# Kernel tuning notes

Hardware: AMD Instinct MI355X
Metric: run time of the kernel (lower is better)

## Reference

```python
import jax, jax.numpy as jnp
import numpy as np

EPS = 1e-5
DOWNSAMPLE = 0.5


def setup_inputs() -> dict:
    key = jax.random.key(0)
    k1, k2, k3 = jax.random.split(key, 3)
    B, C, H, W = 32, 256, 128, 128
    x = jax.random.normal(k1, (B, C, H, W), dtype=jnp.float32)
    # 1x1 conv: weight [3, C], bias [3]
    conv_w = jax.random.normal(k2, (3, C), dtype=jnp.float32) / np.sqrt(C).astype(np.float32)
    conv_b = jax.random.normal(k3, (3,), dtype=jnp.float32) * 0.01
    return {"x": x, "conv_w": conv_w, "conv_b": conv_b}


def reference(x, conv_w, conv_b):
    B, C, H, W = x.shape
    dh = int(round(H * DOWNSAMPLE))
    dw = int(round(W * DOWNSAMPLE))

    # 1x1 conv producing 3 channels: 2 offset + 1 attention logit
    oa = jnp.einsum('bchw,oc->bohw', x, conv_w) + conv_b[None, :, None, None]
    offset = oa[:, :2]                      # [B,2,H,W]
    attention = jnp.exp(oa[:, 2:3])         # [B,1,H,W]

    # normalized destination coordinates = base grid + offset, clamped
    gy = jnp.broadcast_to((jnp.arange(H, dtype=x.dtype) / H)[:, None], (H, W))
    gx = jnp.broadcast_to((jnp.arange(W, dtype=x.dtype) / W)[None, :], (H, W))
    base = jnp.stack([gy, gx])              # [2,H,W]
    dest = jnp.clip(base[None] + offset, 0.0, 1.0 - EPS)
    dy = jnp.floor(dest[:, 0] * dh)
    dx = jnp.floor(dest[:, 1] * dw)
    cell = (dy * dw + dx).astype(jnp.int32)  # [B,H,W] spatial cell index

    # full flat destination index over (batch, channel, cell)
    b_off = jnp.arange(B, dtype=jnp.int32)[:, None, None, None] * (C * dh * dw)
    c_off = jnp.arange(C, dtype=jnp.int32)[None, :, None, None] * (dh * dw)
    destination = cell[:, None] + b_off + c_off  # [B,C,H,W]

    # scatter-add attention-weighted features
    xw = (x * attention).reshape(-1)
    feat = jax.ops.segment_sum(xw, destination.reshape(-1), num_segments=B * C * dh * dw)

    # scatter-add attention per (batch, cell) for normalization
    a_idx = cell + jnp.arange(B, dtype=jnp.int32)[:, None, None] * (dh * dw)
    att_sum = jax.ops.segment_sum(attention.reshape(-1), a_idx.reshape(-1), num_segments=B * dh * dw) + EPS

    out = feat.reshape(B, C, dh, dw) / att_sum.reshape(B, 1, dh, dw)
    return (out, offset, destination)
```

## Files before the change

kernel.cpp:

```cpp
#include <hip/hip_runtime.h>
#include <math.h>

#define NB 32
#define NC 256
#define NH 128
#define NW 128
#define NDH 64
#define NDW 64
#define NHW (NH * NW)
#define NCELLS (NDH * NDW)
#define OUT0_N (NB * NC * NCELLS)
#define OUT1_BASE OUT0_N
#define OUT1_N (NB * 2 * NHW)
#define OUT2_BASE (OUT1_BASE + OUT1_N)

#define EPSF 1e-5f

typedef unsigned short u16;
typedef unsigned int   u32;

#define WS_CELLS     ((size_t)0)
#define WS_ATTBF     (WS_CELLS + (size_t)NB*NHW*2)
#define WS_ECOMB     (WS_ATTBF + (size_t)NB*NHW*2)
#define WS_IASUM     (WS_ECOMB + (size_t)NB*NHW*4)
#define WS_BASE_NEED (WS_IASUM + (size_t)NB*NCELLS*4)
#define WS_XATT      WS_BASE_NEED
#define WS_XATT_NEED (WS_XATT + (size_t)NB*NC*NHW*2)

__device__ __forceinline__ u16 f32_to_bf16_rn(float f) {
    const u32 u = __float_as_uint(f);
    return (u16)((u + 0x7FFFu + ((u >> 16) & 1u)) >> 16);
}

__device__ __forceinline__ void async_stage16(const void* g, void* l) {
    __builtin_amdgcn_global_load_lds(
        (const __attribute__((address_space(1))) unsigned int*)g,
        (__attribute__((address_space(3))) unsigned int*)l,
        16, 0, 0);
}

__global__ __launch_bounds__(256) void k_conv_x(
    const float* __restrict__ x, const float* __restrict__ cw,
    const float* __restrict__ cb, float* __restrict__ out,
    u16* __restrict__ cells, u16* __restrict__ attbf, u16* __restrict__ xatt)
{
    __shared__ float cwS[3][NC];
    __shared__ float red[256][13];
    __shared__ float attv[64];
    __shared__ int   cellv[64];

    const int t    = threadIdx.x;
    const int blk  = blockIdx.x;
    const int b    = blk >> 8;
    const int tile = blk & 255;
    const int h    = tile >> 1;
    const int w0   = (tile & 1) << 6;
    const int pixbase = h * NW + w0;

    cwS[0][t] = cw[t];
    cwS[1][t] = cw[NC + t];
    cwS[2][t] = cw[2 * NC + t];
    __syncthreads();

    const int ct = t >> 4;
    const int pg = (t & 15) << 2;
    const float* xb = x + (size_t)b * NC * NHW + pixbase + pg;

    float4 xr[16];
    float p00 = 0, p01 = 0, p02 = 0;
    float p10 = 0, p11 = 0, p12 = 0;
    float p20 = 0, p21 = 0, p22 = 0;
    float p30 = 0, p31 = 0, p32 = 0;

    #pragma unroll
    for (int i = 0; i < 16; ++i) {
        const int c = (i << 4) + ct;
        const float4 xv = *reinterpret_cast<const float4*>(xb + (size_t)c * NHW);
        xr[i] = xv;
        const float wc0 = cwS[0][c], wc1 = cwS[1][c], wc2 = cwS[2][c];
        p00 += xv.x * wc0; p01 += xv.x * wc1; p02 += xv.x * wc2;
        p10 += xv.y * wc0; p11 += xv.y * wc1; p12 += xv.y * wc2;
        p20 += xv.z * wc0; p21 += xv.z * wc1; p22 += xv.z * wc2;
        p30 += xv.w * wc0; p31 += xv.w * wc1; p32 += xv.w * wc2;
    }

    red[t][0]  = p00; red[t][1]  = p01; red[t][2]  = p02;
    red[t][3]  = p10; red[t][4]  = p11; red[t][5]  = p12;
    red[t][6]  = p20; red[t][7]  = p21; red[t][8]  = p22;
    red[t][9]  = p30; red[t][10] = p31; red[t][11] = p32;
    __syncthreads();

    if (t < 64) {
        const int px   = t;
        const int row0 = px >> 2;
        const int col  = (px & 3) * 3;
        float s0 = 0, s1 = 0, s2 = 0;
        #pragma unroll
        for (int j = 0; j < 16; ++j) {
            const int r = row0 + (j << 4);
            s0 += red[r][col];
            s1 += red[r][col + 1];
            s2 += red[r][col + 2];
        }
        const float off0 = s0 + cb[0];
        const float off1 = s1 + cb[1];
        const float att  = expf(s2 + cb[2]);

        const float gy = (float)h * (1.0f / NH);
        const float gx = (float)(w0 + px) * (1.0f / NW);
        const float dyf = fminf(fmaxf(gy + off0, 0.0f), 0.99999f);
        const float dxf = fminf(fmaxf(gx + off1, 0.0f), 0.99999f);
        const int dy = (int)floorf(dyf * (float)NDH);
        const int dx = (int)floorf(dxf * (float)NDW);
        const int cell = dy * NDW + dx;

        cellv[px] = cell;
        attv[px]  = att;
        cells[b * NHW + pixbase + px] = (u16)cell;
        attbf[b * NHW + pixbase + px] = f32_to_bf16_rn(att);

        const int o1 = OUT1_BASE + b * 2 * NHW + pixbase + px;
        out[o1]       = off0;
        out[o1 + NHW] = off1;
    }
    __syncthreads();

    const int  c0 = cellv[pg], c1 = cellv[pg + 1], c2 = cellv[pg + 2], c3 = cellv[pg + 3];
    const float a0 = attv[pg], a1 = attv[pg + 1], a2 = attv[pg + 2], a3 = attv[pg + 3];
    float* __restrict__ dst = out + OUT2_BASE;

    #pragma unroll
    for (int i = 0; i < 16; ++i) {
        const int c = (i << 4) + ct;
        const int basec = (b * NC + c) * NCELLS;
        float4 dv;
        dv.x = (float)(basec + c0);
        dv.y = (float)(basec + c1);
        dv.z = (float)(basec + c2);
        dv.w = (float)(basec + c3);
        *reinterpret_cast<float4*>(dst + (size_t)(b * NC + c) * NHW + pixbase + pg) = dv;

        const float4 xv = xr[i];
        const u32 lo = (u32)f32_to_bf16_rn(xv.x * a0)
                     | ((u32)f32_to_bf16_rn(xv.y * a1) << 16);
        const u32 hi = (u32)f32_to_bf16_rn(xv.z * a2)
                     | ((u32)f32_to_bf16_rn(xv.w * a3) << 16);
        *reinterpret_cast<uint2*>(xatt + (size_t)(b * NC + c) * NHW + pixbase + pg)
            = make_uint2(lo, hi);
    }
}

__global__ __launch_bounds__(256) void k_conv(
    const float* __restrict__ x, const float* __restrict__ cw,
    const float* __restrict__ cb, float* __restrict__ out,
    u16* __restrict__ cells, u16* __restrict__ attbf)
{
    __shared__ float cwS[3][NC];
    __shared__ float red[256][13];
    __shared__ int   cellv[64];

    const int t    = threadIdx.x;
    const int blk  = blockIdx.x;
    const int b    = blk >> 8;
    const int tile = blk & 255;
    const int h    = tile >> 1;
    const int w0   = (tile & 1) << 6;
    const int pixbase = h * NW + w0;

    cwS[0][t] = cw[t];
    cwS[1][t] = cw[NC + t];
    cwS[2][t] = cw[2 * NC + t];
    __syncthreads();

    const int ct = t >> 4;
    const int pg = (t & 15) << 2;
    const float* xb = x + (size_t)b * NC * NHW + pixbase + pg;

    float p00 = 0, p01 = 0, p02 = 0;
    float p10 = 0, p11 = 0, p12 = 0;
    float p20 = 0, p21 = 0, p22 = 0;
    float p30 = 0, p31 = 0, p32 = 0;

    #pragma unroll
    for (int i = 0; i < 16; ++i) {
        const int c = (i << 4) + ct;
        const float4 xv = *reinterpret_cast<const float4*>(xb + (size_t)c * NHW);
        const float wc0 = cwS[0][c], wc1 = cwS[1][c], wc2 = cwS[2][c];
        p00 += xv.x * wc0; p01 += xv.x * wc1; p02 += xv.x * wc2;
        p10 += xv.y * wc0; p11 += xv.y * wc1; p12 += xv.y * wc2;
        p20 += xv.z * wc0; p21 += xv.z * wc1; p22 += xv.z * wc2;
        p30 += xv.w * wc0; p31 += xv.w * wc1; p32 += xv.w * wc2;
    }

    red[t][0]  = p00; red[t][1]  = p01; red[t][2]  = p02;
    red[t][3]  = p10; red[t][4]  = p11; red[t][5]  = p12;
    red[t][6]  = p20; red[t][7]  = p21; red[t][8]  = p22;
    red[t][9]  = p30; red[t][10] = p31; red[t][11] = p32;
    __syncthreads();

    if (t < 64) {
        const int px   = t;
        const int row0 = px >> 2;
        const int col  = (px & 3) * 3;
        float s0 = 0, s1 = 0, s2 = 0;
        #pragma unroll
        for (int j = 0; j < 16; ++j) {
            const int r = row0 + (j << 4);
            s0 += red[r][col];
            s1 += red[r][col + 1];
            s2 += red[r][col + 2];
        }
        const float off0 = s0 + cb[0];
        const float off1 = s1 + cb[1];
        const float att  = expf(s2 + cb[2]);
        const float gy = (float)h * (1.0f / NH);
        const float gx = (float)(w0 + px) * (1.0f / NW);
        const float dyf = fminf(fmaxf(gy + off0, 0.0f), 0.99999f);
        const float dxf = fminf(fmaxf(gx + off1, 0.0f), 0.99999f);
        const int dy = (int)floorf(dyf * (float)NDH);
        const int dx = (int)floorf(dxf * (float)NDW);
        const int cell = dy * NDW + dx;
        cellv[px] = cell;
        cells[b * NHW + pixbase + px] = (u16)cell;
        attbf[b * NHW + pixbase + px] = f32_to_bf16_rn(att);
        const int o1 = OUT1_BASE + b * 2 * NHW + pixbase + px;
        out[o1]       = off0;
        out[o1 + NHW] = off1;
    }
    __syncthreads();

    const int  c0 = cellv[pg], c1 = cellv[pg + 1], c2 = cellv[pg + 2], c3 = cellv[pg + 3];
    float* __restrict__ dst = out + OUT2_BASE;
    #pragma unroll
    for (int i = 0; i < 16; ++i) {
        const int c = (i << 4) + ct;
        const int basec = (b * NC + c) * NCELLS;
        float4 dv;
        dv.x = (float)(basec + c0);
        dv.y = (float)(basec + c1);
        dv.z = (float)(basec + c2);
        dv.w = (float)(basec + c3);
        *reinterpret_cast<float4*>(dst + (size_t)(b * NC + c) * NHW + pixbase + pg) = dv;
    }
}

__global__ __launch_bounds__(1024) void k_sort(
    const u16* __restrict__ cells, const u16* __restrict__ attbf,
    u32* __restrict__ ecomb, float* __restrict__ iasum)
{
    __shared__ u32   hist[NCELLS];
    __shared__ float as_[NCELLS];
    __shared__ u32   ts[1024];

    const int t = threadIdx.x;
    const int b = blockIdx.x;
    const u16* cb_ = cells + b * NHW;
    const u16* ab_ = attbf + b * NHW;

    #pragma unroll
    for (int j = 0; j < 4; ++j) { hist[t + 1024 * j] = 0u; as_[t + 1024 * j] = 0.f; }
    __syncthreads();

    #pragma unroll
    for (int j = 0; j < 16; ++j) {
        const int p  = t + 1024 * j;
        const int cl = cb_[p];
        atomicAdd(&hist[cl], 1u);
        atomicAdd(&as_[cl], __uint_as_float((u32)ab_[p] << 16));
    }
    __syncthreads();

    const u32 h0 = hist[4 * t], h1 = hist[4 * t + 1], h2 = hist[4 * t + 2], h3 = hist[4 * t + 3];
    const u32 T  = h0 + h1 + h2 + h3;
    ts[t] = T;
    __syncthreads();
    for (int off = 1; off < 1024; off <<= 1) {
        const u32 v = (t >= off) ? ts[t - off] : 0u;
        __syncthreads();
        ts[t] += v;
        __syncthreads();
    }
    const u32 base = ts[t] - T;
    hist[4 * t]     = base;
    hist[4 * t + 1] = base + h0;
    hist[4 * t + 2] = base + h0 + h1;
    hist[4 * t + 3] = base + h0 + h1 + h2;

    #pragma unroll
    for (int j = 0; j < 4; ++j) {
        const int i = t + 1024 * j;
        iasum[b * NCELLS + i] = 1.0f / (as_[i] + EPSF);
    }
    __syncthreads();

    #pragma unroll
    for (int j = 0; j < 16; ++j) {
        const int p  = t + 1024 * j;
        const int cl = cb_[p];
        const u32 pos = atomicAdd(&hist[cl], 1u);
        ecomb[b * NHW + pos] = ((u32)cl << 16) | (u32)p;
    }
}

#define BF16V(E) __uint_as_float((u32)xpl[(E) & 0xFFFFu] << 16)
#define ACCUM(CUR, S, E, V)                                                   \
    {                                                                         \
        const int cl_ = (int)((E) >> 16);                                     \
        if (cl_ != (CUR)) { atomicAdd(&acc[(CUR)], (S)); (S) = 0.f; (CUR) = cl_; } \
        (S) += (V);                                                           \
    }

__device__ __forceinline__ void gather_core(
    const u16* __restrict__ xpl, float* __restrict__ acc,
    const u32* __restrict__ el)
{
    float s0 = 0.f, s1 = 0.f, s2 = 0.f, s3 = 0.f;
    int   c0 = (int)(el[0]  >> 16);
    int   c1 = (int)(el[8]  >> 16);
    int   c2 = (int)(el[16] >> 16);
    int   c3 = (int)(el[24] >> 16);

    #pragma unroll
    for (int ch = 0; ch < 2; ++ch) {
        const uint4 e0 = *reinterpret_cast<const uint4*>(el + ch * 4);
        const uint4 e1 = *reinterpret_cast<const uint4*>(el + 8  + ch * 4);
        const uint4 e2 = *reinterpret_cast<const uint4*>(el + 16 + ch * 4);
        const uint4 e3 = *reinterpret_cast<const uint4*>(el + 24 + ch * 4);
        const float v00 = BF16V(e0.x), v01 = BF16V(e0.y), v02 = BF16V(e0.z), v03 = BF16V(e0.w);
        const float v10 = BF16V(e1.x), v11 = BF16V(e1.y), v12 = BF16V(e1.z), v13 = BF16V(e1.w);
        const float v20 = BF16V(e2.x), v21 = BF16V(e2.y), v22 = BF16V(e2.z), v23 = BF16V(e2.w);
        const float v30 = BF16V(e3.x), v31 = BF16V(e3.y), v32 = BF16V(e3.z), v33 = BF16V(e3.w);
        ACCUM(c0, s0, e0.x, v00); ACCUM(c1, s1, e1.x, v10); ACCUM(c2, s2, e2.x, v20); ACCUM(c3, s3, e3.x, v30);
        ACCUM(c0, s0, e0.y, v01); ACCUM(c1, s1, e1.y, v11); ACCUM(c2, s2, e2.y, v21); ACCUM(c3, s3, e3.y, v31);
        ACCUM(c0, s0, e0.z, v02); ACCUM(c1, s1, e1.z, v12); ACCUM(c2, s2, e2.z, v22); ACCUM(c3, s3, e3.z, v32);
        ACCUM(c0, s0, e0.w, v03); ACCUM(c1, s1, e1.w, v13); ACCUM(c2, s2, e2.w, v23); ACCUM(c3, s3, e3.w, v33);
    }
    atomicAdd(&acc[c0], s0);
    atomicAdd(&acc[c1], s1);
    atomicAdd(&acc[c2], s2);
    atomicAdd(&acc[c3], s3);
}

__global__ __launch_bounds__(512, 6) void k_gather_x(
    const u16* __restrict__ xatt, const u32* __restrict__ ecomb,
    const float* __restrict__ iasum, float* __restrict__ out)
{
    __shared__ u16   xpl[NHW];
    __shared__ float acc[NCELLS];

    const int t    = threadIdx.x;
    const int blk  = blockIdx.x;
    const int b    = blk >> 8;
    const int c    = blk & 255;
    const int wave = t >> 6;
    const int lane = t & 63;

    const u16* xp = xatt + (size_t)(b * NC + c) * NHW;
    #pragma unroll
    for (int k = 0; k < 4; ++k) {
        const int chunk = wave * 4 + k;
        const int e0    = chunk * 512;
        async_stage16(xp + e0 + lane * 8, &xpl[e0 + lane * 8]);
    }

    float4* acc4 = reinterpret_cast<float4*>(acc);
    const float4 z4 = make_float4(0.f, 0.f, 0.f, 0.f);
    #pragma unroll
    for (int k = 0; k < 2; ++k) acc4[t + 512 * k] = z4;
    __syncthreads();

    gather_core(xpl, acc, ecomb + b * NHW + t * 32);
    __syncthreads();

    const float4* ia4 = reinterpret_cast<const float4*>(iasum + b * NCELLS);
    float4* ob4 = reinterpret_cast<float4*>(out + (size_t)(b * NC + c) * NCELLS);
    #pragma unroll
    for (int k = 0; k < 2; ++k) {
        float4 a = acc4[t + 512 * k];
        const float4 sv = ia4[t + 512 * k];
        a.x *= sv.x;
        a.y *= sv.y;
        a.z *= sv.z;
        a.w *= sv.w;
        ob4[t + 512 * k] = a;
    }
}

__global__ __launch_bounds__(512, 6) void k_gather(
    const float* __restrict__ x, const u16* __restrict__ attbf,
    const u32* __restrict__ ecomb, const float* __restrict__ iasum,
    float* __restrict__ out)
{
    __shared__ u16   xpl[NHW];
    __shared__ float acc[NCELLS];

    const int t   = threadIdx.x;
    const int blk = blockIdx.x;
    const int b   = blk >> 8;
    const int c   = blk & 255;

    const float4* xp4 = reinterpret_cast<const float4*>(x + (size_t)(b * NC + c) * NHW);
    const uint2*  ab2 = reinterpret_cast<const uint2*>(attbf + (size_t)b * NHW);
    float4*       acc4 = reinterpret_cast<float4*>(acc);

    #pragma unroll
    for (int k = 0; k < 8; ++k) {
        const int idx = t + 512 * k;
        const float4 xv = xp4[idx];
        const uint2  av = ab2[idx];
        const float a0 = __uint_as_float((u32)av.x << 16);
        const float a1 = __uint_as_float(av.x & 0xFFFF0000u);
        const float a2 = __uint_as_float((u32)av.y << 16);
        const float a3 = __uint_as_float(av.y & 0xFFFF0000u);
        const u32 lo = (u32)f32_to_bf16_rn(xv.x * a0)
                     | ((u32)f32_to_bf16_rn(xv.y * a1) << 16);
        const u32 hi = (u32)f32_to_bf16_rn(xv.z * a2)
                     | ((u32)f32_to_bf16_rn(xv.w * a3) << 16);
        *reinterpret_cast<uint2*>(&xpl[idx * 4]) = make_uint2(lo, hi);
    }
    const float4 z4 = make_float4(0.f, 0.f, 0.f, 0.f);
    #pragma unroll
    for (int k = 0; k < 2; ++k) acc4[t + 512 * k] = z4;
    __syncthreads();

    gather_core(xpl, acc, ecomb + b * NHW + t * 32);
    __syncthreads();

    const float4* ia4 = reinterpret_cast<const float4*>(iasum + b * NCELLS);
    float4* ob4 = reinterpret_cast<float4*>(out + (size_t)(b * NC + c) * NCELLS);
    #pragma unroll
    for (int k = 0; k < 2; ++k) {
        float4 a = acc4[t + 512 * k];
        const float4 sv = ia4[t + 512 * k];
        a.x *= sv.x;
        a.y *= sv.y;
        a.z *= sv.z;
        a.w *= sv.w;
        ob4[t + 512 * k] = a;
    }
}

extern "C" void kernel_launch(void* const* d_in, const int* in_sizes, int n_in,
                              void* d_out, int out_size, void* d_ws, size_t ws_size,
                              hipStream_t stream)
{
    (void)in_sizes; (void)n_in; (void)out_size;
    const float* x  = (const float*)d_in[0];
    const float* cw = (const float*)d_in[1];
    const float* cb = (const float*)d_in[2];
    float* out = (float*)d_out;
    char*  ws  = (char*)d_ws;

    u16*   cells = (u16*)  (ws + WS_CELLS);
    u16*   attbf = (u16*)  (ws + WS_ATTBF);
    u32*   ecomb = (u32*)  (ws + WS_ECOMB);
    float* iasum = (float*)(ws + WS_IASUM);

    if (ws_size >= WS_XATT_NEED) {
        u16* xatt = (u16*)(ws + WS_XATT);
        k_conv_x  <<<dim3(NB * 256), dim3(256),  0, stream>>>(x, cw, cb, out, cells, attbf, xatt);
        k_sort    <<<dim3(NB),       dim3(1024), 0, stream>>>(cells, attbf, ecomb, iasum);
        k_gather_x<<<dim3(NB * NC),  dim3(512),  0, stream>>>(xatt, ecomb, iasum, out);
    } else {
        k_conv  <<<dim3(NB * 256), dim3(256),  0, stream>>>(x, cw, cb, out, cells, attbf);
        k_sort  <<<dim3(NB),       dim3(1024), 0, stream>>>(cells, attbf, ecomb, iasum);
        k_gather<<<dim3(NB * NC),  dim3(512),  0, stream>>>(x, attbf, ecomb, iasum, out);
    }
}
```

Before: 492.8 us.

## Quantize attention-weighted intermediate to FP8 and prefetch sorted indices into registers

The conv kernel now writes the attention-weighted x intermediate as a custom FP8 (e4m3-like) byte instead of bf16, halving the traffic for writing and re-reading this large buffer. The gather kernel decodes FP8 back to bf16 in LDS, and it preloads the sorted index list into registers before staging. Other changes: nontemporal stores for the large destination and output writes, the batch processing order reversed in gather to improve cache reuse of the sort results, and the occupancy hint on launch bounds dropped. FP8 quantization loses precision and flushes values below 2^-6 to zero, which may break accuracy tolerance.

```diff
diff --git a/kernel.cpp b/kernel.cpp
--- a/kernel.cpp
+++ b/kernel.cpp
@@ -24,25 +24,40 @@
 #define WS_ECOMB     (WS_ATTBF + (size_t)NB*NHW*2)
 #define WS_IASUM     (WS_ECOMB + (size_t)NB*NHW*4)
 #define WS_BASE_NEED (WS_IASUM + (size_t)NB*NCELLS*4)
-#define WS_XATT      WS_BASE_NEED
-#define WS_XATT_NEED (WS_XATT + (size_t)NB*NC*NHW*2)
+#define WS_XQ        WS_BASE_NEED
+#define WS_XQ_NEED   (WS_XQ + (size_t)NB*NC*NHW)
 
 __device__ __forceinline__ u16 f32_to_bf16_rn(float f) {
     const u32 u = __float_as_uint(f);
     return (u16)((u + 0x7FFFu + ((u >> 16) & 1u)) >> 16);
 }
 
-__device__ __forceinline__ void async_stage16(const void* g, void* l) {
-    __builtin_amdgcn_global_load_lds(
-        (const __attribute__((address_space(1))) unsigned int*)g,
-        (__attribute__((address_space(3))) unsigned int*)l,
-        16, 0, 0);
-}
-
-__global__ __launch_bounds__(256) void k_conv_x(
+__device__ __forceinline__ u32 f32_to_fp8(float f) {
+    const u32 s = (__float_as_uint(f) >> 24) & 0x80u;
+    float a = fabsf(f);
+    a = fminf(a, 448.0f);
+    const u32 b = __float_as_uint(a) + 0x00080000u;
+    const u32 r = s | (((b >> 23) - 120u) << 3) | ((b >> 20) & 7u);
+    return (a >= 0.015625f) ? r : s;
+}
+
+__device__ __forceinline__ u32 fp8_to_bf16(u32 v) {
+    const u32 m = v & 0x7Fu;
+    const u32 bf = ((v & 0x80u) << 8) | ((m + 0x3C0u) << 4);
+    return m ? bf : ((v & 0x80u) << 8);
+}
+
+__device__ __forceinline__ void store_nt4(float* p, float4 v) {
+    __builtin_nontemporal_store(v.x, p);
+    __builtin_nontemporal_store(v.y, p + 1);
+    __builtin_nontemporal_store(v.z, p + 2);
+    __builtin_nontemporal_store(v.w, p + 3);
+}
+
+__global__ __launch_bounds__(256) void k_conv_q(
     const float* __restrict__ x, const float* __restrict__ cw,
     const float* __restrict__ cb, float* __restrict__ out,
-    u16* __restrict__ cells, u16* __restrict__ attbf, u16* __restrict__ xatt)
+    u16* __restrict__ cells, u16* __restrict__ attbf, unsigned char* __restrict__ xq)
 {
     __shared__ float cwS[3][NC];
     __shared__ float red[256][13];
@@ -138,15 +153,14 @@
         dv.y = (float)(basec + c1);
         dv.z = (float)(basec + c2);
         dv.w = (float)(basec + c3);
-        *reinterpret_cast<float4*>(dst + (size_t)(b * NC + c) * NHW + pixbase + pg) = dv;
+        store_nt4(dst + (size_t)(b * NC + c) * NHW + pixbase + pg, dv);
 
         const float4 xv = xr[i];
-        const u32 lo = (u32)f32_to_bf16_rn(xv.x * a0)
-                     | ((u32)f32_to_bf16_rn(xv.y * a1) << 16);
-        const u32 hi = (u32)f32_to_bf16_rn(xv.z * a2)
-                     | ((u32)f32_to_bf16_rn(xv.w * a3) << 16);
-        *reinterpret_cast<uint2*>(xatt + (size_t)(b * NC + c) * NHW + pixbase + pg)
-            = make_uint2(lo, hi);
+        const u32 q = f32_to_fp8(xv.x * a0)
+                    | (f32_to_fp8(xv.y * a1) << 8)
+                    | (f32_to_fp8(xv.z * a2) << 16)
+                    | (f32_to_fp8(xv.w * a3) << 24);
+        *reinterpret_cast<u32*>(xq + (size_t)(b * NC + c) * NHW + pixbase + pg) = q;
     }
 }
 
@@ -240,7 +254,7 @@
         dv.y = (float)(basec + c1);
         dv.z = (float)(basec + c2);
         dv.w = (float)(basec + c3);
-        *reinterpret_cast<float4*>(dst + (size_t)(b * NC + c) * NHW + pixbase + pg) = dv;
+        store_nt4(dst + (size_t)(b * NC + c) * NHW + pixbase + pg, dv);
     }
 }
 
@@ -310,22 +324,21 @@
         (S) += (V);                                                           \
     }
 
-__device__ __forceinline__ void gather_core(
-    const u16* __restrict__ xpl, float* __restrict__ acc,
-    const u32* __restrict__ el)
+__device__ __forceinline__ void gather_core_q(
+    const u16* __restrict__ xpl, float* __restrict__ acc, const uint4* q)
 {
     float s0 = 0.f, s1 = 0.f, s2 = 0.f, s3 = 0.f;
-    int   c0 = (int)(el[0]  >> 16);
-    int   c1 = (int)(el[8]  >> 16);
-    int   c2 = (int)(el[16] >> 16);
-    int   c3 = (int)(el[24] >> 16);
+    int   c0 = (int)(q[0].x >> 16);
+    int   c1 = (int)(q[2].x >> 16);
+    int   c2 = (int)(q[4].x >> 16);
+    int   c3 = (int)(q[6].x >> 16);
 
     #pragma unroll
     for (int ch = 0; ch < 2; ++ch) {
-        const uint4 e0 = *reinterpret_cast<const uint4*>(el + ch * 4);
-        const uint4 e1 = *reinterpret_cast<const uint4*>(el + 8  + ch * 4);
-        const uint4 e2 = *reinterpret_cast<const uint4*>(el + 16 + ch * 4);
-        const uint4 e3 = *reinterpret_cast<const uint4*>(el + 24 + ch * 4);
+        const uint4 e0 = q[ch];
+        const uint4 e1 = q[2 + ch];
+        const uint4 e2 = q[4 + ch];
+        const uint4 e3 = q[6 + ch];
         const float v00 = BF16V(e0.x), v01 = BF16V(e0.y), v02 = BF16V(e0.z), v03 = BF16V(e0.w);
         const float v10 = BF16V(e1.x), v11 = BF16V(e1.y), v12 = BF16V(e1.z), v13 = BF16V(e1.w);
         const float v20 = BF16V(e2.x), v21 = BF16V(e2.y), v22 = BF16V(e2.z), v23 = BF16V(e2.w);
@@ -341,52 +354,59 @@
     atomicAdd(&acc[c3], s3);
 }
 
-__global__ __launch_bounds__(512, 6) void k_gather_x(
-    const u16* __restrict__ xatt, const u32* __restrict__ ecomb,
+__global__ __launch_bounds__(512) void k_gather_q(
+    const unsigned char* __restrict__ xq, const u32* __restrict__ ecomb,
     const float* __restrict__ iasum, float* __restrict__ out)
 {
     __shared__ u16   xpl[NHW];
     __shared__ float acc[NCELLS];
 
-    const int t    = threadIdx.x;
-    const int blk  = blockIdx.x;
-    const int b    = blk >> 8;
-    const int c    = blk & 255;
-    const int wave = t >> 6;
-    const int lane = t & 63;
-
-    const u16* xp = xatt + (size_t)(b * NC + c) * NHW;
-    #pragma unroll
-    for (int k = 0; k < 4; ++k) {
-        const int chunk = wave * 4 + k;
-        const int e0    = chunk * 512;
-        async_stage16(xp + e0 + lane * 8, &xpl[e0 + lane * 8]);
-    }
-
+    const int t   = threadIdx.x;
+    const int blk = blockIdx.x;
+    const int b   = (NB - 1) - (blk >> 8);
+    const int c   = blk & 255;
+
+    const u32* el = ecomb + b * NHW + t * 32;
+    uint4 q[8];
+    #pragma unroll
+    for (int i = 0; i < 8; ++i)
+        q[i] = *reinterpret_cast<const uint4*>(el + i * 4);
+
+    const u32* xq32 = reinterpret_cast<const u32*>(xq + (size_t)(b * NC + c) * NHW);
     float4* acc4 = reinterpret_cast<float4*>(acc);
+
+    #pragma unroll
+    for (int k = 0; k < 8; ++k) {
+        const int i = t + 512 * k;
+        const u32 w = xq32[i];
+        const u32 b0 = fp8_to_bf16(w & 0xFFu);
+        const u32 b1 = fp8_to_bf16((w >> 8) & 0xFFu);
+        const u32 b2 = fp8_to_bf16((w >> 16) & 0xFFu);
+        const u32 b3 = fp8_to_bf16(w >> 24);
+        *reinterpret_cast<uint2*>(&xpl[i * 4]) =
+            make_uint2(b0 | (b1 << 16), b2 | (b3 << 16));
+    }
     const float4 z4 = make_float4(0.f, 0.f, 0.f, 0.f);
     #pragma unroll
     for (int k = 0; k < 2; ++k) acc4[t + 512 * k] = z4;
     __syncthreads();
 
-    gather_core(xpl, acc, ecomb + b * NHW + t * 32);
-    __syncthreads();
+    gather_core_q(xpl, acc, q);
 
     const float4* ia4 = reinterpret_cast<const float4*>(iasum + b * NCELLS);
+    const float4 i0 = ia4[t], i1 = ia4[t + 512];
+    __syncthreads();
+
     float4* ob4 = reinterpret_cast<float4*>(out + (size_t)(b * NC + c) * NCELLS);
-    #pragma unroll
-    for (int k = 0; k < 2; ++k) {
-        float4 a = acc4[t + 512 * k];
-        const float4 sv = ia4[t + 512 * k];
-        a.x *= sv.x;
-        a.y *= sv.y;
-        a.z *= sv.z;
-        a.w *= sv.w;
-        ob4[t + 512 * k] = a;
-    }
-}
-
-__global__ __launch_bounds__(512, 6) void k_gather(
+    float4 a0 = acc4[t];
+    float4 a1 = acc4[t + 512];
+    a0.x *= i0.x; a0.y *= i0.y; a0.z *= i0.z; a0.w *= i0.w;
+    a1.x *= i1.x; a1.y *= i1.y; a1.z *= i1.z; a1.w *= i1.w;
+    store_nt4(reinterpret_cast<float*>(ob4 + t), a0);
+    store_nt4(reinterpret_cast<float*>(ob4 + t + 512), a1);
+}
+
+__global__ __launch_bounds__(512) void k_gather(
     const float* __restrict__ x, const u16* __restrict__ attbf,
     const u32* __restrict__ ecomb, const float* __restrict__ iasum,
     float* __restrict__ out)
@@ -396,8 +416,14 @@
 
     const int t   = threadIdx.x;
     const int blk = blockIdx.x;
-    const int b   = blk >> 8;
+    const int b   = (NB - 1) - (blk >> 8);
     const int c   = blk & 255;
+
+    const u32* el = ecomb + b * NHW + t * 32;
+    uint4 q[8];
+    #pragma unroll
+    for (int i = 0; i < 8; ++i)
+        q[i] = *reinterpret_cast<const uint4*>(el + i * 4);
 
     const float4* xp4 = reinterpret_cast<const float4*>(x + (size_t)(b * NC + c) * NHW);
     const uint2*  ab2 = reinterpret_cast<const uint2*>(attbf + (size_t)b * NHW);
@@ -423,21 +449,19 @@
     for (int k = 0; k < 2; ++k) acc4[t + 512 * k] = z4;
     __syncthreads();
 
-    gather_core(xpl, acc, ecomb + b * NHW + t * 32);
-    __syncthreads();
+    gather_core_q(xpl, acc, q);
 
     const float4* ia4 = reinterpret_cast<const float4*>(iasum + b * NCELLS);
+    const float4 i0 = ia4[t], i1 = ia4[t + 512];
+    __syncthreads();
+
     float4* ob4 = reinterpret_cast<float4*>(out + (size_t)(b * NC + c) * NCELLS);
-    #pragma unroll
-    for (int k = 0; k < 2; ++k) {
-        float4 a = acc4[t + 512 * k];
-        const float4 sv = ia4[t + 512 * k];
-        a.x *= sv.x;
-        a.y *= sv.y;
-        a.z *= sv.z;
-        a.w *= sv.w;
-        ob4[t + 512 * k] = a;
-    }
+    float4 a0 = acc4[t];
+    float4 a1 = acc4[t + 512];
+    a0.x *= i0.x; a0.y *= i0.y; a0.z *= i0.z; a0.w *= i0.w;
+    a1.x *= i1.x; a1.y *= i1.y; a1.z *= i1.z; a1.w *= i1.w;
+    store_nt4(reinterpret_cast<float*>(ob4 + t), a0);
+    store_nt4(reinterpret_cast<float*>(ob4 + t + 512), a1);
 }
 
 extern "C" void kernel_launch(void* const* d_in, const int* in_sizes, int n_in,
@@ -456,11 +480,11 @@
     u32*   ecomb = (u32*)  (ws + WS_ECOMB);
     float* iasum = (float*)(ws + WS_IASUM);
 
-    if (ws_size >= WS_XATT_NEED) {
-        u16* xatt = (u16*)(ws + WS_XATT);
-        k_conv_x  <<<dim3(NB * 256), dim3(256),  0, stream>>>(x, cw, cb, out, cells, attbf, xatt);
+    if (ws_size >= WS_XQ_NEED) {
+        unsigned char* xq = (unsigned char*)(ws + WS_XQ);
+        k_conv_q  <<<dim3(NB * 256), dim3(256),  0, stream>>>(x, cw, cb, out, cells, attbf, xq);
         k_sort    <<<dim3(NB),       dim3(1024), 0, stream>>>(cells, attbf, ecomb, iasum);
-        k_gather_x<<<dim3(NB * NC),  dim3(512),  0, stream>>>(xatt, ecomb, iasum, out);
+        k_gather_q<<<dim3(NB * NC),  dim3(512),  0, stream>>>(xq, ecomb, iasum, out);
     } else {
         k_conv  <<<dim3(NB * 256), dim3(256),  0, stream>>>(x, cw, cb, out, cells, attbf);
         k_sort  <<<dim3(NB),       dim3(1024), 0, stream>>>(cells, attbf, ecomb, iasum);
```

New measurement: 467.0 us. 1.06x faster.
